# Kernel optimization log

Measured on AMD Instinct MI355X. Metric: run time of the kernel, lower is better.

## Reference

```python
import jax, jax.numpy as jnp
import numpy as np

B, S, H, DH = 2, 4096, 8, 64
D = H * DH


def setup_inputs() -> dict:
    key = jax.random.key(0)
    ks = jax.random.split(key, 6)
    std = 1.0 / np.sqrt(D)
    return {
        "x": jax.random.normal(ks[0], (B, S, D), dtype=jnp.float32),
        "Wq": jax.random.normal(ks[1], (D, D), dtype=jnp.float32) * std,
        "Wk": jax.random.normal(ks[2], (D, D), dtype=jnp.float32) * std,
        "Wv": jax.random.normal(ks[3], (D, D), dtype=jnp.float32) * std,
        "Wo": jax.random.normal(ks[4], (D, D), dtype=jnp.float32) * std,
        "bo": jnp.zeros((D,), dtype=jnp.float32),
    }


def reference(x, Wq, Wk, Wv, Wo, bo):
    scale = DH ** (-0.5)
    # torch Linear: y = x @ W.T
    q = x @ Wq.T  # [B,S,D]
    k = x @ Wk.T
    v = x @ Wv.T
    # split heads -> [B,H,S,Dh]
    q = q.reshape(B, S, H, DH).transpose(0, 2, 1, 3)
    k = k.reshape(B, S, H, DH).transpose(0, 2, 1, 3)
    v = v.reshape(B, S, H, DH).transpose(0, 2, 1, 3)
    score = jnp.einsum('bhqd,bhkd->bhqk', q, k) * scale  # [B,H,S,S]
    weights = jax.nn.softmax(score, axis=-1)
    attn = jnp.einsum('bhqk,bhkd->bhqd', weights, v)  # [B,H,S,Dh]
    h_ = attn.transpose(0, 2, 1, 3).reshape(B, S, D)
    return h_ @ Wo.T + bo
```

## Files before the change

kernel.cpp:

```cpp
#include <hip/hip_runtime.h>

#define LOG2E 1.44269504088896340736f

typedef unsigned short u16;
typedef __bf16 bf16x4_t __attribute__((ext_vector_type(4)));
typedef __bf16 bf16x8_t __attribute__((ext_vector_type(8)));
typedef float f32x4_t __attribute__((ext_vector_type(4)));

__device__ __forceinline__ u16 f2bf(float f) {
  union { float f; unsigned int u; } v;
  v.f = f;
  unsigned int u = v.u;
  u += 0x7fffu + ((u >> 16) & 1u);
  return (u16)(u >> 16);
}

__device__ __forceinline__ f32x4_t mfma16(bf16x8_t a, bf16x8_t b, f32x4_t c) {
  return __builtin_amdgcn_mfma_f32_16x16x32_bf16(a, b, c, 0, 0, 0);
}

__device__ __forceinline__ void gl_lds16(const u16* g, u16* l) {
  __builtin_amdgcn_global_load_lds(
      (const __attribute__((address_space(1))) unsigned int*)g,
      (__attribute__((address_space(3))) unsigned int*)l, 16, 0, 0);
}

__global__ __launch_bounds__(256) void cast_all_kernel(
    const float* __restrict__ x, const float* __restrict__ wq, const float* __restrict__ wk,
    const float* __restrict__ wv, const float* __restrict__ wo,
    u16* __restrict__ xb, u16* __restrict__ wqb, u16* __restrict__ wkb,
    u16* __restrict__ wvb, u16* __restrict__ wob) {
  const int NX = 2 * 4096 * 512;
  const int NW = 512 * 512;
  int i = (blockIdx.x * 256 + threadIdx.x) * 4;
  const float* src; u16* dst; int off; float scale = 1.f;
  if (i < NX)               { src = x;  dst = xb;  off = i; }
  else if (i < NX + NW)     { src = wq; dst = wqb; off = i - NX; scale = 0.125f * LOG2E; }
  else if (i < NX + 2 * NW) { src = wk; dst = wkb; off = i - NX - NW; }
  else if (i < NX + 3 * NW) { src = wv; dst = wvb; off = i - NX - 2 * NW; }
  else                      { src = wo; dst = wob; off = i - NX - 3 * NW; }
  float4 f = *(const float4*)(src + off);
  unsigned int lo = (unsigned int)f2bf(f.x * scale) | ((unsigned int)f2bf(f.y * scale) << 16);
  unsigned int hi = (unsigned int)f2bf(f.z * scale) | ((unsigned int)f2bf(f.w * scale) << 16);
  uint2 o; o.x = lo; o.y = hi;
  *(uint2*)(dst + off) = o;
}

template <int MODE>
__device__ __forceinline__ void gemm_core(const u16* __restrict__ A, const u16* __restrict__ Bt,
                                          void* __restrict__ Cout, const float* __restrict__ bias,
                                          int Mbase, int Nbase) {
  __shared__ __align__(16) u16 As[128][40];
  __shared__ __align__(16) u16 Bs[128][40];
  const int t = threadIdx.x;
  const int wave = t >> 6, lane = t & 63;
  const int r = lane & 15, qd = lane >> 4;
  const int wm = wave & 1, wn = wave >> 1;
  const int lr = t >> 2;
  const int lc = (t & 3) * 8;

  f32x4_t acc[4][4];
#pragma unroll
  for (int i = 0; i < 4; i++)
#pragma unroll
    for (int j = 0; j < 4; j++) { f32x4_t z = {0.f, 0.f, 0.f, 0.f}; acc[i][j] = z; }

  const u16* pa0 = A  + (Mbase + lr) * 512 + lc;
  const u16* pa1 = A  + (Mbase + 64 + lr) * 512 + lc;
  const u16* pb0 = Bt + (Nbase + lr) * 512 + lc;
  const u16* pb1 = Bt + (Nbase + 64 + lr) * 512 + lc;

  uint4 ra0 = *(const uint4*)(pa0);
  uint4 ra1 = *(const uint4*)(pa1);
  uint4 rb0 = *(const uint4*)(pb0);
  uint4 rb1 = *(const uint4*)(pb1);

  for (int k0 = 0; k0 < 512; k0 += 32) {
    *(uint4*)&As[lr][lc]      = ra0;
    *(uint4*)&As[64 + lr][lc] = ra1;
    *(uint4*)&Bs[lr][lc]      = rb0;
    *(uint4*)&Bs[64 + lr][lc] = rb1;
    __syncthreads();
    if (k0 < 480) {
      ra0 = *(const uint4*)(pa0 + k0 + 32);
      ra1 = *(const uint4*)(pa1 + k0 + 32);
      rb0 = *(const uint4*)(pb0 + k0 + 32);
      rb1 = *(const uint4*)(pb1 + k0 + 32);
    }
    bf16x8_t af[4], bfr[4];
#pragma unroll
    for (int i = 0; i < 4; i++) af[i]  = *(const bf16x8_t*)&As[wm * 64 + i * 16 + r][qd * 8];
#pragma unroll
    for (int j = 0; j < 4; j++) bfr[j] = *(const bf16x8_t*)&Bs[wn * 64 + j * 16 + r][qd * 8];
#pragma unroll
    for (int i = 0; i < 4; i++)
#pragma unroll
      for (int j = 0; j < 4; j++) acc[i][j] = mfma16(af[i], bfr[j], acc[i][j]);
    __syncthreads();
  }

  float bv[4];
  if (MODE == 2) {
#pragma unroll
    for (int j = 0; j < 4; j++) bv[j] = bias[Nbase + wn * 64 + j * 16 + r];
  }
#pragma unroll
  for (int i = 0; i < 4; i++) {
#pragma unroll
    for (int reg = 0; reg < 4; reg++) {
      int gr = Mbase + wm * 64 + i * 16 + qd * 4 + reg;
#pragma unroll
      for (int j = 0; j < 4; j++) {
        int gc = Nbase + wn * 64 + j * 16 + r;
        float val = acc[i][j][reg];
        if (MODE == 2) {
          ((float*)Cout)[gr * 512 + gc] = val + bv[j];
        } else if (MODE == 1) {
          int bb = gc >> 12, ss = gc & 4095;
          ((__bf16*)Cout)[((long)(bb * 512 + gr)) * 4096 + ss] = (__bf16)val;
        } else {
          ((__bf16*)Cout)[gr * 512 + gc] = (__bf16)val;
        }
      }
    }
  }
}

__global__ __launch_bounds__(256) void gemm_qkv_kernel(
    const u16* __restrict__ X,
    const u16* __restrict__ Wq, const u16* __restrict__ Wk, const u16* __restrict__ Wv,
    u16* __restrict__ Q, u16* __restrict__ K, u16* __restrict__ Vt) {
  if (blockIdx.z == 0)
    gemm_core<0>(X, Wq, Q, nullptr, blockIdx.x * 128, blockIdx.y * 128);
  else if (blockIdx.z == 1)
    gemm_core<0>(X, Wk, K, nullptr, blockIdx.x * 128, blockIdx.y * 128);
  else
    gemm_core<1>(Wv, X, Vt, nullptr, blockIdx.y * 128, blockIdx.x * 128);
}

__global__ __launch_bounds__(256) void gemm_out_kernel(
    const u16* __restrict__ Aat, const u16* __restrict__ Wo,
    float* __restrict__ Out, const float* __restrict__ bo) {
  gemm_core<2>(Aat, Wo, Out, bo, blockIdx.x * 128, blockIdx.y * 128);
}

__global__ __launch_bounds__(256, 2) void attn_kernel(
    const u16* __restrict__ Q, const u16* __restrict__ K, const u16* __restrict__ Vt,
    u16* __restrict__ Oattn) {
  __shared__ __align__(16) u16 Ks[2][2][4096];
  __shared__ __align__(16) u16 Vs[2][2][4096];

  const int t = threadIdx.x;
  const int wave = t >> 6, lane = t & 63;
  const int r = lane & 15, qd = lane >> 4;
  const int g = wave & 1, kv = wave >> 1;
  const int bh = blockIdx.y;
  const int b = bh >> 3, h = bh & 7;
  const long bbase = (long)b * 4096 * 512;
  const int q0 = blockIdx.x * 128;

  const int sw = r & 7;
  const int ck0 = (qd ^ sw) * 8;
  const int ck1 = ((qd + 4) ^ sw) * 8;
  int vo0[2], vo1[2];
#pragma unroll
  for (int c = 0; c < 2; c++) {
    vo0[c] = ((c * 4 + (qd >> 1)) ^ sw) * 8 + 4 * (qd & 1);
    vo1[c] = ((c * 4 + 2 + (qd >> 1)) ^ sw) * 8 + 4 * (qd & 1);
  }

  bf16x8_t ones8;
#pragma unroll
  for (int j = 0; j < 8; j++) ones8[j] = (__bf16)1.0f;

  bf16x8_t qf[4][2];
#pragma unroll
  for (int qa = 0; qa < 4; qa++) {
    const u16* qp = Q + bbase + (long)(q0 + g * 64 + qa * 16 + r) * 512 + h * 64 + qd * 8;
    qf[qa][0] = *(const bf16x8_t*)(qp);
    qf[qa][1] = *(const bf16x8_t*)(qp + 32);
  }

  f32x4_t accO[4][4];
  f32x4_t accL[4];
#pragma unroll
  for (int qa = 0; qa < 4; qa++) {
    f32x4_t z = {0.f, 0.f, 0.f, 0.f};
    accL[qa] = z;
#pragma unroll
    for (int nt = 0; nt < 4; nt++) accO[qa][nt] = z;
  }

  const int rr = lane >> 3;
  const int cc = (lane & 7) ^ rr;
  const u16* kgb = K + bbase + (long)(kv * 2048 + g * 32 + rr) * 512 + h * 64 + cc * 8;
  const u16* vgb = Vt + ((long)(b * 512 + h * 64 + g * 32 + rr)) * 4096 + kv * 2048 + cc * 8;

#pragma unroll
  for (int i = 0; i < 4; i++) gl_lds16(kgb + (long)i * 8 * 512, &Ks[kv][0][g * 2048] + i * 512);
#pragma unroll
  for (int i = 0; i < 4; i++) gl_lds16(vgb + i * 8 * 4096, &Vs[kv][0][g * 2048] + i * 512);

  for (int it = 0; it < 32; it++) {
    const int buf = it & 1;
    __syncthreads();

    if (it < 31) {
      const int nb = (it + 1) & 1;
      const long ko = (long)(it + 1) * 64;
#pragma unroll
      for (int i = 0; i < 4; i++)
        gl_lds16(kgb + (ko + i * 8) * 512, &Ks[kv][nb][g * 2048] + i * 512);
#pragma unroll
      for (int i = 0; i < 4; i++)
        gl_lds16(vgb + ko + (long)i * 8 * 4096, &Vs[kv][nb][g * 2048] + i * 512);
    }

    bf16x8_t kf[4][2];
#pragma unroll
    for (int nt = 0; nt < 4; nt++) {
      const u16* kb = &Ks[kv][buf][(nt * 16 + r) * 64];
      kf[nt][0] = *(const bf16x8_t*)(kb + ck0);
      kf[nt][1] = *(const bf16x8_t*)(kb + ck1);
    }

    f32x4_t St[4][4];
#pragma unroll
    for (int qa = 0; qa < 4; qa++)
#pragma unroll
      for (int nt = 0; nt < 4; nt++) {
        f32x4_t z = {0.f, 0.f, 0.f, 0.f};
        z = mfma16(kf[nt][0], qf[qa][0], z);
        z = mfma16(kf[nt][1], qf[qa][1], z);
        St[qa][nt] = z;
      }

    bf16x8_t pf[4][2];
#pragma unroll
    for (int qa = 0; qa < 4; qa++)
#pragma unroll
      for (int c = 0; c < 2; c++) {
        f32x4_t e0, e1;
#pragma unroll
        for (int j = 0; j < 4; j++) {
          e0[j] = __builtin_amdgcn_exp2f(St[qa][2 * c][j]);
          e1[j] = __builtin_amdgcn_exp2f(St[qa][2 * c + 1][j]);
        }
        bf16x4_t b0 = __builtin_convertvector(e0, bf16x4_t);
        bf16x4_t b1 = __builtin_convertvector(e1, bf16x4_t);
        bf16x8_t p8;
#pragma unroll
        for (int j = 0; j < 4; j++) { p8[j] = b0[j]; p8[4 + j] = b1[j]; }
        pf[qa][c] = p8;
      }

#pragma unroll
    for (int qa = 0; qa < 4; qa++)
#pragma unroll
      for (int c = 0; c < 2; c++)
        accL[qa] = mfma16(ones8, pf[qa][c], accL[qa]);

#pragma unroll
    for (int c = 0; c < 2; c++) {
      bf16x8_t va[4];
#pragma unroll
      for (int dm = 0; dm < 4; dm++) {
        const u16* vb = &Vs[kv][buf][(dm * 16 + r) * 64];
        union { uint4 u; bf16x8_t v; } cat;
        *(uint2*)&cat.u.x = *(const uint2*)(vb + vo0[c]);
        *(uint2*)&cat.u.z = *(const uint2*)(vb + vo1[c]);
        va[dm] = cat.v;
      }
#pragma unroll
      for (int qa = 0; qa < 4; qa++)
#pragma unroll
        for (int dm = 0; dm < 4; dm++)
          accO[qa][dm] = mfma16(va[dm], pf[qa][c], accO[qa][dm]);
    }
  }

  __syncthreads();
  float* Sc  = (float*)&Ks[0][0][0];
  float* Lsc = (float*)&Vs[0][0][0];
  if (kv == 1) {
#pragma unroll
    for (int qa = 0; qa < 4; qa++) {
#pragma unroll
      for (int dm = 0; dm < 4; dm++)
        *(f32x4_t*)&Sc[g * 4096 + ((qa * 4 + dm) * 64 + lane) * 4] = accO[qa][dm];
      Lsc[g * 256 + qa * 64 + lane] = accL[qa][0];
    }
  }
  __syncthreads();
  if (kv == 0) {
#pragma unroll
    for (int qa = 0; qa < 4; qa++) {
      float L = accL[qa][0] + Lsc[g * 256 + qa * 64 + lane];
      float inv = 1.f / L;
      int gq = q0 + g * 64 + qa * 16 + r;
#pragma unroll
      for (int dm = 0; dm < 4; dm++) {
        f32x4_t o = *(const f32x4_t*)&Sc[g * 4096 + ((qa * 4 + dm) * 64 + lane) * 4];
        o += accO[qa][dm];
        bf16x4_t ob;
#pragma unroll
        for (int reg = 0; reg < 4; reg++) ob[reg] = (__bf16)(o[reg] * inv);
        *(uint2*)&Oattn[bbase + (long)gq * 512 + h * 64 + dm * 16 + qd * 4] = *(uint2*)&ob;
      }
    }
  }
}

extern "C" void kernel_launch(void* const* d_in, const int* in_sizes, int n_in,
                              void* d_out, int out_size, void* d_ws, size_t ws_size,
                              hipStream_t stream) {
  const float* x  = (const float*)d_in[0];
  const float* Wq = (const float*)d_in[1];
  const float* Wk = (const float*)d_in[2];
  const float* Wv = (const float*)d_in[3];
  const float* Wo = (const float*)d_in[4];
  const float* bo = (const float*)d_in[5];
  float* out = (float*)d_out;

  u16* ws  = (u16*)d_ws;
  u16* xb  = ws;
  u16* wqb = xb  + 4194304;
  u16* wkb = wqb + 262144;
  u16* wvb = wkb + 262144;
  u16* wob = wvb + 262144;
  u16* Qb  = wob + 262144;
  u16* Kb  = Qb  + 4194304;
  u16* Vtg = Kb  + 4194304;
  u16* Ab  = Vtg + 4194304;

  cast_all_kernel<<<5120, 256, 0, stream>>>(x, Wq, Wk, Wv, Wo, xb, wqb, wkb, wvb, wob);

  dim3 g1(64, 4, 3);
  gemm_qkv_kernel<<<g1, 256, 0, stream>>>(xb, wqb, wkb, wvb, Qb, Kb, Vtg);

  dim3 g2(32, 16);
  attn_kernel<<<g2, 256, 0, stream>>>(Qb, Kb, Vtg, Ab);

  dim3 g3(64, 4);
  gemm_out_kernel<<<g3, 256, 0, stream>>>(Ab, wob, out, bo);
}
```

Measured before the change: 191.9 us.

## Fuse fp32-to-bf16 casts into GEMM loads and retile output projection

Removes the standalone cast kernel. The QKV GEMM now loads fp32 x and weights directly, converts them to bf16 when writing to LDS, and applies the Q scale there. The output GEMM reads Wo as fp32 and uses 64-row tiles to double the grid to 128x4 blocks. This saves one launch and the bf16 intermediate round trip. The cost is double the global load bytes per tile for fp32 inputs, and x is re-read and converted once per N block.

```diff
diff --git a/kernel.cpp b/kernel.cpp
--- a/kernel.cpp
+++ b/kernel.cpp
@@ -7,14 +7,6 @@
 typedef __bf16 bf16x8_t __attribute__((ext_vector_type(8)));
 typedef float f32x4_t __attribute__((ext_vector_type(4)));
 
-__device__ __forceinline__ u16 f2bf(float f) {
-  union { float f; unsigned int u; } v;
-  v.f = f;
-  unsigned int u = v.u;
-  u += 0x7fffu + ((u >> 16) & 1u);
-  return (u16)(u >> 16);
-}
-
 __device__ __forceinline__ f32x4_t mfma16(bf16x8_t a, bf16x8_t b, f32x4_t c) {
   return __builtin_amdgcn_mfma_f32_16x16x32_bf16(a, b, c, 0, 0, 0);
 }
@@ -25,31 +17,18 @@
       (__attribute__((address_space(3))) unsigned int*)l, 16, 0, 0);
 }
 
-__global__ __launch_bounds__(256) void cast_all_kernel(
-    const float* __restrict__ x, const float* __restrict__ wq, const float* __restrict__ wk,
-    const float* __restrict__ wv, const float* __restrict__ wo,
-    u16* __restrict__ xb, u16* __restrict__ wqb, u16* __restrict__ wkb,
-    u16* __restrict__ wvb, u16* __restrict__ wob) {
-  const int NX = 2 * 4096 * 512;
-  const int NW = 512 * 512;
-  int i = (blockIdx.x * 256 + threadIdx.x) * 4;
-  const float* src; u16* dst; int off; float scale = 1.f;
-  if (i < NX)               { src = x;  dst = xb;  off = i; }
-  else if (i < NX + NW)     { src = wq; dst = wqb; off = i - NX; scale = 0.125f * LOG2E; }
-  else if (i < NX + 2 * NW) { src = wk; dst = wkb; off = i - NX - NW; }
-  else if (i < NX + 3 * NW) { src = wv; dst = wvb; off = i - NX - 2 * NW; }
-  else                      { src = wo; dst = wob; off = i - NX - 3 * NW; }
-  float4 f = *(const float4*)(src + off);
-  unsigned int lo = (unsigned int)f2bf(f.x * scale) | ((unsigned int)f2bf(f.y * scale) << 16);
-  unsigned int hi = (unsigned int)f2bf(f.z * scale) | ((unsigned int)f2bf(f.w * scale) << 16);
-  uint2 o; o.x = lo; o.y = hi;
-  *(uint2*)(dst + off) = o;
+__device__ __forceinline__ void cvt_store(u16* dst, f32x4_t a, f32x4_t b, float scale) {
+  a *= scale; b *= scale;
+  union { uint4 u; struct { bf16x4_t lo, hi; } s; } c;
+  c.s.lo = __builtin_convertvector(a, bf16x4_t);
+  c.s.hi = __builtin_convertvector(b, bf16x4_t);
+  *(uint4*)dst = c.u;
 }
 
 template <int MODE>
-__device__ __forceinline__ void gemm_core(const u16* __restrict__ A, const u16* __restrict__ Bt,
-                                          void* __restrict__ Cout, const float* __restrict__ bias,
-                                          int Mbase, int Nbase) {
+__device__ __forceinline__ void gemm_core_f32(const float* __restrict__ A, const float* __restrict__ Bt,
+                                              u16* __restrict__ Cout, int Mbase, int Nbase,
+                                              float bscale) {
   __shared__ __align__(16) u16 As[128][40];
   __shared__ __align__(16) u16 Bs[128][40];
   const int t = threadIdx.x;
@@ -65,27 +44,28 @@
 #pragma unroll
     for (int j = 0; j < 4; j++) { f32x4_t z = {0.f, 0.f, 0.f, 0.f}; acc[i][j] = z; }
 
-  const u16* pa0 = A  + (Mbase + lr) * 512 + lc;
-  const u16* pa1 = A  + (Mbase + 64 + lr) * 512 + lc;
-  const u16* pb0 = Bt + (Nbase + lr) * 512 + lc;
-  const u16* pb1 = Bt + (Nbase + 64 + lr) * 512 + lc;
-
-  uint4 ra0 = *(const uint4*)(pa0);
-  uint4 ra1 = *(const uint4*)(pa1);
-  uint4 rb0 = *(const uint4*)(pb0);
-  uint4 rb1 = *(const uint4*)(pb1);
+  const float* pa0 = A  + (Mbase + lr) * 512 + lc;
+  const float* pa1 = A  + (Mbase + 64 + lr) * 512 + lc;
+  const float* pb0 = Bt + (Nbase + lr) * 512 + lc;
+  const float* pb1 = Bt + (Nbase + 64 + lr) * 512 + lc;
+
+  f32x4_t ra0[2], ra1[2], rb0[2], rb1[2];
+  ra0[0] = *(const f32x4_t*)(pa0); ra0[1] = *(const f32x4_t*)(pa0 + 4);
+  ra1[0] = *(const f32x4_t*)(pa1); ra1[1] = *(const f32x4_t*)(pa1 + 4);
+  rb0[0] = *(const f32x4_t*)(pb0); rb0[1] = *(const f32x4_t*)(pb0 + 4);
+  rb1[0] = *(const f32x4_t*)(pb1); rb1[1] = *(const f32x4_t*)(pb1 + 4);
 
   for (int k0 = 0; k0 < 512; k0 += 32) {
-    *(uint4*)&As[lr][lc]      = ra0;
-    *(uint4*)&As[64 + lr][lc] = ra1;
-    *(uint4*)&Bs[lr][lc]      = rb0;
-    *(uint4*)&Bs[64 + lr][lc] = rb1;
+    cvt_store(&As[lr][lc],      ra0[0], ra0[1], 1.f);
+    cvt_store(&As[64 + lr][lc], ra1[0], ra1[1], 1.f);
+    cvt_store(&Bs[lr][lc],      rb0[0], rb0[1], bscale);
+    cvt_store(&Bs[64 + lr][lc], rb1[0], rb1[1], bscale);
     __syncthreads();
     if (k0 < 480) {
-      ra0 = *(const uint4*)(pa0 + k0 + 32);
-      ra1 = *(const uint4*)(pa1 + k0 + 32);
-      rb0 = *(const uint4*)(pb0 + k0 + 32);
-      rb1 = *(const uint4*)(pb1 + k0 + 32);
+      ra0[0] = *(const f32x4_t*)(pa0 + k0 + 32); ra0[1] = *(const f32x4_t*)(pa0 + k0 + 36);
+      ra1[0] = *(const f32x4_t*)(pa1 + k0 + 32); ra1[1] = *(const f32x4_t*)(pa1 + k0 + 36);
+      rb0[0] = *(const f32x4_t*)(pb0 + k0 + 32); rb0[1] = *(const f32x4_t*)(pb0 + k0 + 36);
+      rb1[0] = *(const f32x4_t*)(pb1 + k0 + 32); rb1[1] = *(const f32x4_t*)(pb1 + k0 + 36);
     }
     bf16x8_t af[4], bfr[4];
 #pragma unroll
@@ -99,11 +79,6 @@
     __syncthreads();
   }
 
-  float bv[4];
-  if (MODE == 2) {
-#pragma unroll
-    for (int j = 0; j < 4; j++) bv[j] = bias[Nbase + wn * 64 + j * 16 + r];
-  }
 #pragma unroll
   for (int i = 0; i < 4; i++) {
 #pragma unroll
@@ -113,9 +88,7 @@
       for (int j = 0; j < 4; j++) {
         int gc = Nbase + wn * 64 + j * 16 + r;
         float val = acc[i][j][reg];
-        if (MODE == 2) {
-          ((float*)Cout)[gr * 512 + gc] = val + bv[j];
-        } else if (MODE == 1) {
+        if (MODE == 1) {
           int bb = gc >> 12, ss = gc & 4095;
           ((__bf16*)Cout)[((long)(bb * 512 + gr)) * 4096 + ss] = (__bf16)val;
         } else {
@@ -127,21 +100,81 @@
 }
 
 __global__ __launch_bounds__(256) void gemm_qkv_kernel(
-    const u16* __restrict__ X,
-    const u16* __restrict__ Wq, const u16* __restrict__ Wk, const u16* __restrict__ Wv,
+    const float* __restrict__ X,
+    const float* __restrict__ Wq, const float* __restrict__ Wk, const float* __restrict__ Wv,
     u16* __restrict__ Q, u16* __restrict__ K, u16* __restrict__ Vt) {
   if (blockIdx.z == 0)
-    gemm_core<0>(X, Wq, Q, nullptr, blockIdx.x * 128, blockIdx.y * 128);
+    gemm_core_f32<0>(X, Wq, Q, blockIdx.x * 128, blockIdx.y * 128, 0.125f * LOG2E);
   else if (blockIdx.z == 1)
-    gemm_core<0>(X, Wk, K, nullptr, blockIdx.x * 128, blockIdx.y * 128);
+    gemm_core_f32<0>(X, Wk, K, blockIdx.x * 128, blockIdx.y * 128, 1.f);
   else
-    gemm_core<1>(Wv, X, Vt, nullptr, blockIdx.y * 128, blockIdx.x * 128);
+    gemm_core_f32<1>(Wv, X, Vt, blockIdx.y * 128, blockIdx.x * 128, 1.f);
 }
 
 __global__ __launch_bounds__(256) void gemm_out_kernel(
-    const u16* __restrict__ Aat, const u16* __restrict__ Wo,
+    const u16* __restrict__ Aat, const float* __restrict__ Wo,
     float* __restrict__ Out, const float* __restrict__ bo) {
-  gemm_core<2>(Aat, Wo, Out, bo, blockIdx.x * 128, blockIdx.y * 128);
+  __shared__ __align__(16) u16 As[64][40];
+  __shared__ __align__(16) u16 Bs[128][40];
+  const int t = threadIdx.x;
+  const int wave = t >> 6, lane = t & 63;
+  const int r = lane & 15, qd = lane >> 4;
+  const int wn = wave;
+  const int Mbase = blockIdx.x * 64, Nbase = blockIdx.y * 128;
+  const int lr = t >> 2;
+  const int lc = (t & 3) * 8;
+
+  f32x4_t acc[4][2];
+#pragma unroll
+  for (int i = 0; i < 4; i++)
+#pragma unroll
+    for (int j = 0; j < 2; j++) { f32x4_t z = {0.f, 0.f, 0.f, 0.f}; acc[i][j] = z; }
+
+  const u16*  pa  = Aat + (Mbase + lr) * 512 + lc;
+  const float* pb0 = Wo + (Nbase + lr) * 512 + lc;
+  const float* pb1 = Wo + (Nbase + 64 + lr) * 512 + lc;
+
+  uint4 ra = *(const uint4*)(pa);
+  f32x4_t rb0[2], rb1[2];
+  rb0[0] = *(const f32x4_t*)(pb0); rb0[1] = *(const f32x4_t*)(pb0 + 4);
+  rb1[0] = *(const f32x4_t*)(pb1); rb1[1] = *(const f32x4_t*)(pb1 + 4);
+
+  for (int k0 = 0; k0 < 512; k0 += 32) {
+    *(uint4*)&As[lr][lc] = ra;
+    cvt_store(&Bs[lr][lc],      rb0[0], rb0[1], 1.f);
+    cvt_store(&Bs[64 + lr][lc], rb1[0], rb1[1], 1.f);
+    __syncthreads();
+    if (k0 < 480) {
+      ra = *(const uint4*)(pa + k0 + 32);
+      rb0[0] = *(const f32x4_t*)(pb0 + k0 + 32); rb0[1] = *(const f32x4_t*)(pb0 + k0 + 36);
+      rb1[0] = *(const f32x4_t*)(pb1 + k0 + 32); rb1[1] = *(const f32x4_t*)(pb1 + k0 + 36);
+    }
+    bf16x8_t af[4], bfr[2];
+#pragma unroll
+    for (int i = 0; i < 4; i++) af[i]  = *(const bf16x8_t*)&As[i * 16 + r][qd * 8];
+#pragma unroll
+    for (int j = 0; j < 2; j++) bfr[j] = *(const bf16x8_t*)&Bs[wn * 32 + j * 16 + r][qd * 8];
+#pragma unroll
+    for (int i = 0; i < 4; i++)
+#pragma unroll
+      for (int j = 0; j < 2; j++) acc[i][j] = mfma16(af[i], bfr[j], acc[i][j]);
+    __syncthreads();
+  }
+
+  float bv[2];
+#pragma unroll
+  for (int j = 0; j < 2; j++) bv[j] = bo[Nbase + wn * 32 + j * 16 + r];
+#pragma unroll
+  for (int i = 0; i < 4; i++)
+#pragma unroll
+    for (int reg = 0; reg < 4; reg++) {
+      int gr = Mbase + i * 16 + qd * 4 + reg;
+#pragma unroll
+      for (int j = 0; j < 2; j++) {
+        int gc = Nbase + wn * 32 + j * 16 + r;
+        Out[gr * 512 + gc] = acc[i][j][reg] + bv[j];
+      }
+    }
 }
 
 __global__ __launch_bounds__(256, 2) void attn_kernel(
@@ -323,24 +356,17 @@
   float* out = (float*)d_out;
 
   u16* ws  = (u16*)d_ws;
-  u16* xb  = ws;
-  u16* wqb = xb  + 4194304;
-  u16* wkb = wqb + 262144;
-  u16* wvb = wkb + 262144;
-  u16* wob = wvb + 262144;
-  u16* Qb  = wob + 262144;
+  u16* Qb  = ws;
   u16* Kb  = Qb  + 4194304;
   u16* Vtg = Kb  + 4194304;
   u16* Ab  = Vtg + 4194304;
 
-  cast_all_kernel<<<5120, 256, 0, stream>>>(x, Wq, Wk, Wv, Wo, xb, wqb, wkb, wvb, wob);
-
   dim3 g1(64, 4, 3);
-  gemm_qkv_kernel<<<g1, 256, 0, stream>>>(xb, wqb, wkb, wvb, Qb, Kb, Vtg);
+  gemm_qkv_kernel<<<g1, 256, 0, stream>>>(x, Wq, Wk, Wv, Qb, Kb, Vtg);
 
   dim3 g2(32, 16);
   attn_kernel<<<g2, 256, 0, stream>>>(Qb, Kb, Vtg, Ab);
 
-  dim3 g3(64, 4);
-  gemm_out_kernel<<<g3, 256, 0, stream>>>(Ab, wob, out, bo);
-}
+  dim3 g3(128, 4);
+  gemm_out_kernel<<<g3, 256, 0, stream>>>(Ab, Wo, out, bo);
+}
```

After: 187.7 us. 2.2% less time.
